# Kernel tuning notes

Measured on AMD Instinct MI355X. Metric: run time of the kernel, lower is better.

Reference implementation:

```python
import jax, jax.numpy as jnp
import numpy as np

N_HEADS = 16
SEG_LEN = 512
MSG_LEN = 1536
T_TOTAL = SEG_LEN + MSG_LEN  # 2048


def _build_mask(T):
    # rows < SEG_LEN: attend to all cols < SEG_LEN (full, non-causal block)
    # rows >= SEG_LEN: standard causal (cols <= row)
    rows = jnp.arange(T)[:, None]
    cols = jnp.arange(T)[None, :]
    mask = jnp.where(rows < SEG_LEN, cols < SEG_LEN, cols <= rows)
    return mask  # [T, T] bool


def setup_inputs() -> dict:
    key = jax.random.key(0)
    k1, k2, k3 = jax.random.split(key, 3)
    B, T, E = 4, T_TOTAL, 1024
    x = jax.random.normal(k1, (B, T, E), dtype=jnp.float32)
    W_qkv = jax.random.normal(k2, (E, 3 * E), dtype=jnp.float32) * (1.0 / np.sqrt(E))
    b_qkv = jnp.zeros((3 * E,), dtype=jnp.float32)
    W_proj = jax.random.normal(k3, (E, E), dtype=jnp.float32) * (1.0 / np.sqrt(E))
    b_proj = jnp.zeros((E,), dtype=jnp.float32)
    return {"x": x, "W_qkv": W_qkv, "b_qkv": b_qkv, "W_proj": W_proj, "b_proj": b_proj}


def reference(x, W_qkv, b_qkv, W_proj, b_proj):
    B, T, E = x.shape
    H = N_HEADS
    D = E // H
    qkv = x @ W_qkv + b_qkv  # [B, T, 3E]
    q, k, v = jnp.split(qkv, 3, axis=-1)
    # [B, H, T, D]
    q = q.reshape(B, T, H, D).transpose(0, 2, 1, 3)
    k = k.reshape(B, T, H, D).transpose(0, 2, 1, 3)
    v = v.reshape(B, T, H, D).transpose(0, 2, 1, 3)
    att = jnp.einsum("bhqd,bhkd->bhqk", q, k) * (1.0 / np.sqrt(D))
    mask = _build_mask(T)  # [T, T]
    att = jnp.where(mask[None, None], att, jnp.float32(-jnp.inf))
    att = jax.nn.softmax(att, axis=-1)
    y = jnp.einsum("bhqk,bhkd->bhqd", att, v)
    y = y.transpose(0, 2, 1, 3).reshape(B, T, E)
    return y @ W_proj + b_proj
```

## Files before the change

kernel.cpp:

```cpp
#include <hip/hip_runtime.h>


typedef _Float16 f16;
typedef _Float16 f16x4 __attribute__((ext_vector_type(4)));
typedef _Float16 f16x8 __attribute__((ext_vector_type(8)));
typedef float f32x4 __attribute__((ext_vector_type(4)));

#define MFMA16x32(a, b, c) __builtin_amdgcn_mfma_f32_16x16x32_f16(a, b, c, 0, 0, 0)
#define MFMA16x16(a, b, c) __builtin_amdgcn_mfma_f32_16x16x16f16(a, b, c, 0, 0, 0)

__device__ __forceinline__ void gload_lds16(const void* g, void* l) {
  __builtin_amdgcn_global_load_lds(
      (__attribute__((address_space(1))) void*)g,
      (__attribute__((address_space(3))) void*)l, 16, 0, 0);
}


__global__ __launch_bounds__(256) void k_prep(
    const float* __restrict__ x, f16* __restrict__ xh,
    const float* __restrict__ Wq, f16* __restrict__ Wqt,
    const float* __restrict__ Wp, f16* __restrict__ Wpt) {
  __shared__ float tile[32][33];
  const int bid = blockIdx.x;
  if (bid < 8192) {
    int i = bid * 256 + threadIdx.x;
    float4 v = ((const float4*)x)[i];
    f16x4 o = {(f16)v.x, (f16)v.y, (f16)v.z, (f16)v.w};
    ((f16x4*)xh)[i] = o;
    return;
  }
  const float* W;
  f16* Wt;
  int Ndim, bx, by;
  if (bid < 8192 + 3072) {
    int r = bid - 8192;
    W = Wq; Wt = Wqt; Ndim = 3072; bx = r % 96; by = r / 96;
  } else {
    int r = bid - 11264;
    W = Wp; Wt = Wpt; Ndim = 1024; bx = r % 32; by = r / 32;
  }
  const int tx = threadIdx.x & 31, ty = threadIdx.x >> 5;
  const int n = bx * 32 + tx;
  const int k0 = by * 32;
  for (int j = ty; j < 32; j += 8)
    tile[j][tx] = W[(size_t)(k0 + j) * Ndim + n];
  __syncthreads();
  const int k = k0 + tx;
  for (int j = ty; j < 32; j += 8)
    Wt[(size_t)(bx * 32 + j) * 1024 + k] = (f16)tile[tx][j];
}


__global__ __launch_bounds__(512, 2) void k_gemm_qkv(
    const f16* __restrict__ A, const f16* __restrict__ Bt,
    const float* __restrict__ bias,
    f16* __restrict__ Qo, f16* __restrict__ Ko, f16* __restrict__ Vo) {
  constexpr int KD = 1024;
  constexpr int SLOT = (128 + 256) * 64;
  __shared__ __align__(16) f16 smem[3 * SLOT];
  const int tid = threadIdx.x;
  const int wave = tid >> 6, lane = tid & 63;
  const int g = lane >> 4, l16 = lane & 15;
  const int m0 = blockIdx.y * 128, n0 = blockIdx.x * 256;
  const int wm = (wave >> 2) * 64, wn = (wave & 3) * 64;
  const int srow = wave * 8 + (lane >> 3);
  const int skc = ((lane & 7) ^ (lane >> 3)) * 8;

  f32x4 acc[4][4] = {};

  for (int t = 0; t < 2; ++t) {
    f16* Sa = smem + t * SLOT;
    f16* Sb = Sa + 128 * 64;
    for (int it = 0; it < 2; ++it)
      gload_lds16(A + (size_t)(m0 + it * 64 + srow) * KD + t * 64 + skc,
                  Sa + (it * 64 + wave * 8) * 64);
    for (int it = 0; it < 4; ++it)
      gload_lds16(Bt + (size_t)(n0 + it * 64 + srow) * KD + t * 64 + skc,
                  Sb + (it * 64 + wave * 8) * 64);
  }
  asm volatile("s_waitcnt vmcnt(6)" ::: "memory");
  __builtin_amdgcn_s_barrier();

  for (int u = 0; u < 16; ++u) {
    const int s = u % 3;
    f16* Sa = smem + s * SLOT;
    f16* Sb = Sa + 128 * 64;
    const bool pf = (u + 2) < 16;
    f16* Pa = smem + ((u + 2) % 3) * SLOT;
    f16* Pb = Pa + 128 * 64;
    const int kp = (u + 2) * 64;

    for (int kk = 0; kk < 2; ++kk) {
      if (pf) {
        if (kk == 0) {
          gload_lds16(A + (size_t)(m0 + srow) * KD + kp + skc,
                      Pa + (wave * 8) * 64);
          gload_lds16(A + (size_t)(m0 + 64 + srow) * KD + kp + skc,
                      Pa + (64 + wave * 8) * 64);
          gload_lds16(Bt + (size_t)(n0 + srow) * KD + kp + skc,
                      Pb + (wave * 8) * 64);
        } else {
          gload_lds16(Bt + (size_t)(n0 + 64 + srow) * KD + kp + skc,
                      Pb + (64 + wave * 8) * 64);
          gload_lds16(Bt + (size_t)(n0 + 128 + srow) * KD + kp + skc,
                      Pb + (128 + wave * 8) * 64);
          gload_lds16(Bt + (size_t)(n0 + 192 + srow) * KD + kp + skc,
                      Pb + (192 + wave * 8) * 64);
        }
      }

      const int ks = kk * 4;
      f16x8 af[4], bf[4];
      for (int mi = 0; mi < 4; ++mi) {
        int R = wm + mi * 16 + l16, sw = R & 7;
        af[mi] = *(const f16x8*)(Sa + R * 64 + ((ks + g) ^ sw) * 8);
      }
      for (int ni = 0; ni < 4; ++ni) {
        int R = wn + ni * 16 + l16, sw = R & 7;
        bf[ni] = *(const f16x8*)(Sb + R * 64 + ((ks + g) ^ sw) * 8);
      }
      __builtin_amdgcn_s_setprio(1);
      for (int mi = 0; mi < 4; ++mi)
        for (int ni = 0; ni < 4; ++ni)
          acc[mi][ni] = MFMA16x32(af[mi], bf[ni], acc[mi][ni]);
      __builtin_amdgcn_s_setprio(0);
    }

    if (u < 14)
      asm volatile("s_waitcnt vmcnt(6)" ::: "memory");
    else
      asm volatile("s_waitcnt vmcnt(0)" ::: "memory");
    __builtin_amdgcn_s_barrier();
  }

  const int nsub = n0 + wn;
  const int part = nsub >> 10;
  const int h    = (nsub >> 6) & 15;
  const int mg   = m0 + wm;
  const int b    = mg >> 11;
  const int tb   = mg & 2047;
  const size_t bh = (size_t)(b * 16 + h);

  float bv[4];
  for (int ni = 0; ni < 4; ++ni) bv[ni] = bias[nsub + ni * 16 + l16];

  f16* Es = smem + wave * 4096;

  for (int mi = 0; mi < 4; ++mi)
    for (int ni = 0; ni < 4; ++ni)
      for (int r = 0; r < 4; ++r) {
        f16 hv = (f16)(acc[mi][ni][r] + bv[ni]);
        int mrow = mi * 16 + g * 4 + r, ncol = ni * 16 + l16;
        if (part == 2)
          Es[ncol * 64 + (mrow ^ ((ncol & 7) << 3))] = hv;
        else
          Es[mrow * 64 + (ncol ^ ((mrow & 7) << 3))] = hv;
      }

  const int rrow = lane >> 3, rj = lane & 7;
  for (int p = 0; p < 8; ++p) {
    int row = p * 8 + rrow;
    f16x8 vv = *(const f16x8*)(Es + row * 64 + (rj ^ (row & 7)) * 8);
    int rcol = rj * 8;
    if (part == 0)
      *(f16x8*)(Qo + (bh * 2048 + tb + row) * 64 + rcol) = vv;
    else if (part == 1)
      *(f16x8*)(Ko + (bh * 2048 + tb + row) * 64 + rcol) = vv;
    else
      *(f16x8*)(Vo + (bh * 64 + row) * 2048 + tb + rcol) = vv;
  }
}


__global__ __launch_bounds__(256, 4) void k_attn(
    const f16* __restrict__ Q, const f16* __restrict__ Kb,
    const f16* __restrict__ Vt, f16* __restrict__ Y) {
  __shared__ __align__(16) f16 Ks[2][64 * 64];
  __shared__ __align__(16) f16 Vs[2][64 * 64];
  __shared__ float rs[4 * 32];

  const int tid = threadIdx.x;
  const int wave = tid >> 6, lane = tid & 63;
  const int g = lane >> 4, l16 = lane & 15;
  const int bh = blockIdx.x;
  const int b = bh >> 4, h = bh & 15;
  const int qt = 15 - blockIdx.y;
  const int q0 = qt * 128;
  const int nt = (qt < 4) ? 8 : (qt + 1) * 2;
  const int srowrel = lane >> 3;
  const int sc = (lane & 7) ^ srowrel;

  const f32x4 sinit = {-8.65617025f, -8.65617025f, -8.65617025f, -8.65617025f};

  f16x8 aq[2][2];
  for (int mi = 0; mi < 2; ++mi) {
    const f16* qrow =
        Q + ((size_t)bh * 2048 + q0 + wave * 32 + mi * 16 + l16) * 64 + g * 8;
    aq[mi][0] = *(const f16x8*)(qrow);
    aq[mi][1] = *(const f16x8*)(qrow + 32);
    for (int kb = 0; kb < 2; ++kb)
      aq[mi][kb] = aq[mi][kb] * (f16)0.18033688f;
  }

  f32x4 o[2][4] = {};
  float rsum[2] = {};

  for (int it = 0; it < 2; ++it) {
    int row = it * 32 + wave * 8 + srowrel;
    gload_lds16(Kb + ((size_t)bh * 2048 + row) * 64 + sc * 8,
                &Ks[0][(it * 32 + wave * 8) * 64]);
    gload_lds16(Vt + ((size_t)bh * 64 + row) * 2048 + sc * 8,
                &Vs[0][(it * 32 + wave * 8) * 64]);
  }
  __syncthreads();

  int cur = 0;
  for (int i = 0; i < nt; ++i) {
    if (i + 1 < nt) {
      const int kn0 = (i + 1) << 6;
      for (int it = 0; it < 2; ++it) {
        int row = it * 32 + wave * 8 + srowrel;
        gload_lds16(Kb + ((size_t)bh * 2048 + kn0 + row) * 64 + sc * 8,
                    &Ks[cur ^ 1][(it * 32 + wave * 8) * 64]);
        gload_lds16(Vt + ((size_t)bh * 64 + row) * 2048 + kn0 + sc * 8,
                    &Vs[cur ^ 1][(it * 32 + wave * 8) * 64]);
      }
    }

    const int kt0 = i << 6;
    const f16* Kc = Ks[cur];
    const f16* Vc = Vs[cur];

    f32x4 t[2][4];
    __builtin_amdgcn_s_setprio(1);
    for (int nb = 0; nb < 4; ++nb) {
      int R = nb * 16 + l16, sw = R & 7;
      f16x8 bk0 = *(const f16x8*)(Kc + R * 64 + ((0 + g) ^ sw) * 8);
      f16x8 bk1 = *(const f16x8*)(Kc + R * 64 + ((4 + g) ^ sw) * 8);
      for (int mi = 0; mi < 2; ++mi) {
        f32x4 acc = MFMA16x32(bk0, aq[mi][0], sinit);
        t[mi][nb] = MFMA16x32(bk1, aq[mi][1], acc);
      }
    }
    __builtin_amdgcn_s_setprio(0);

    const bool masked = (q0 >= 512) && (kt0 >= q0);
    f16x4 ap[4][2];
    for (int mi = 0; mi < 2; ++mi) {
      const int mrow = q0 + wave * 32 + mi * 16 + l16;
      for (int nb = 0; nb < 4; ++nb)
        for (int r = 0; r < 4; ++r) {
          float pv = __builtin_amdgcn_exp2f(t[mi][nb][r]);
          if (masked && (kt0 + nb * 16 + g * 4 + r > mrow)) pv = 0.f;
          rsum[mi] += pv;
          ap[nb][mi][r] = (f16)pv;
        }
    }

    __builtin_amdgcn_s_setprio(1);
    for (int db = 0; db < 4; ++db)
      for (int nb = 0; nb < 4; ++nb) {
        int R = db * 16 + l16, sw = R & 7;
        int c = nb * 2 + (g >> 1);
        f16x4 bv = *(const f16x4*)(Vc + R * 64 + (c ^ sw) * 8 + (g & 1) * 4);
        for (int mi = 0; mi < 2; ++mi)
          o[mi][db] = MFMA16x16(ap[nb][mi], bv, o[mi][db]);
      }
    __builtin_amdgcn_s_setprio(0);

    __syncthreads();
    cur ^= 1;
  }

  for (int mi = 0; mi < 2; ++mi) {
    rsum[mi] += __shfl_xor(rsum[mi], 16, 64);
    rsum[mi] += __shfl_xor(rsum[mi], 32, 64);
  }

  if (g == 0)
    for (int mi = 0; mi < 2; ++mi) rs[wave * 32 + mi * 16 + l16] = rsum[mi];
  float rinv[2][4];
  for (int mi = 0; mi < 2; ++mi)
    for (int r = 0; r < 4; ++r)
      rinv[mi][r] = 1.0f / rs[wave * 32 + mi * 16 + g * 4 + r];

  const size_t ybase = (size_t)b * 2048 + q0 + wave * 32;
  for (int mi = 0; mi < 2; ++mi)
    for (int db = 0; db < 4; ++db)
      for (int r = 0; r < 4; ++r)
        Y[(ybase + mi * 16 + g * 4 + r) * 1024 + h * 64 + db * 16 + l16] =
            (f16)(o[mi][db][r] * rinv[mi][r]);
}


__global__ __launch_bounds__(256) void k_gemm_proj(
    const f16* __restrict__ A, const f16* __restrict__ Bt,
    const float* __restrict__ bias, float* __restrict__ out) {
  constexpr int KD = 1024;
  __shared__ __align__(16) f16 As[128 * 64];
  __shared__ __align__(16) f16 Bs[128 * 64];
  const int tid = threadIdx.x;
  const int wave = tid >> 6, lane = tid & 63;
  const int g = lane >> 4, l16 = lane & 15;
  const int m0 = blockIdx.y * 128, n0 = blockIdx.x * 128;
  const int wm = (wave >> 1) * 64, wn = (wave & 1) * 64;
  const int srow = wave * 8 + (lane >> 3);
  const int skc = ((lane & 7) ^ (lane >> 3)) * 8;

  f32x4 acc[4][4] = {};

  for (int k0 = 0; k0 < KD; k0 += 64) {
    __syncthreads();
    for (int it = 0; it < 4; ++it) {
      gload_lds16(A + (size_t)(m0 + it * 32 + srow) * KD + k0 + skc,
                  As + (it * 32 + wave * 8) * 64);
      gload_lds16(Bt + (size_t)(n0 + it * 32 + srow) * KD + k0 + skc,
                  Bs + (it * 32 + wave * 8) * 64);
    }
    __syncthreads();
    for (int kk = 0; kk < 64; kk += 32) {
      const int ks = kk >> 3;
      f16x8 af[4], bf[4];
      for (int mi = 0; mi < 4; ++mi) {
        int R = wm + mi * 16 + l16, sw = R & 7;
        af[mi] = *(const f16x8*)(As + R * 64 + ((ks + g) ^ sw) * 8);
      }
      for (int ni = 0; ni < 4; ++ni) {
        int R = wn + ni * 16 + l16, sw = R & 7;
        bf[ni] = *(const f16x8*)(Bs + R * 64 + ((ks + g) ^ sw) * 8);
      }
      for (int mi = 0; mi < 4; ++mi)
        for (int ni = 0; ni < 4; ++ni)
          acc[mi][ni] = MFMA16x32(af[mi], bf[ni], acc[mi][ni]);
    }
  }

  float bv[4];
  for (int ni = 0; ni < 4; ++ni) bv[ni] = bias[n0 + wn + ni * 16 + l16];

  for (int mi = 0; mi < 4; ++mi)
    for (int ni = 0; ni < 4; ++ni)
      for (int r = 0; r < 4; ++r) {
        int m = m0 + wm + mi * 16 + g * 4 + r;
        int n = n0 + wn + ni * 16 + l16;
        out[(size_t)m * 1024 + n] = acc[mi][ni][r] + bv[ni];
      }
}


extern "C" void kernel_launch(void* const* d_in, const int* in_sizes, int n_in,
                              void* d_out, int out_size, void* d_ws,
                              size_t ws_size, hipStream_t stream) {
  const float* x      = (const float*)d_in[0];
  const float* W_qkv  = (const float*)d_in[1];
  const float* b_qkv  = (const float*)d_in[2];
  const float* W_proj = (const float*)d_in[3];
  const float* b_proj = (const float*)d_in[4];
  float* out = (float*)d_out;

  char* ws = (char*)d_ws;
  f16* xh    = (f16*)ws;   ws += (size_t)8192 * 1024 * 2;
  f16* Wqt   = (f16*)ws;   ws += (size_t)3072 * 1024 * 2;
  f16* Wpt   = (f16*)ws;   ws += (size_t)1024 * 1024 * 2;
  f16* Qb    = (f16*)ws;   ws += (size_t)64 * 2048 * 64 * 2;
  f16* Kb    = (f16*)ws;   ws += (size_t)64 * 2048 * 64 * 2;
  f16* Vt    = (f16*)ws;   ws += (size_t)64 * 64 * 2048 * 2;
  f16* Y = xh;

  k_prep<<<12288, 256, 0, stream>>>(x, xh, W_qkv, Wqt, W_proj, Wpt);
  k_gemm_qkv<<<dim3(12, 64), 512, 0, stream>>>(xh, Wqt, b_qkv, Qb, Kb, Vt);
  k_attn<<<dim3(64, 16), 256, 0, stream>>>(Qb, Kb, Vt, Y);
  k_gemm_proj<<<dim3(8, 64), 256, 0, stream>>>(Y, Wpt, b_proj, out);
}
```

Measured before the change: 252.2 us.

## Triple-buffer projection GEMM with larger tiles; compute attention row sums via MFMA

The projection GEMM now uses 512-thread blocks on 128x256 tiles. A three-slot LDS ring prefetches two K-steps ahead, with explicit vmcnt waits and a single barrier per step instead of two syncs per step. This is meant to overlap global loads with MFMA work. In attention, the softmax row sums are computed with an MFMA against a ones vector, which removes the scalar adds, the shuffles and the LDS reduction. The cost is 8 extra MFMAs per tile, plus larger shared memory and register use in the GEMM, which may reduce occupancy.

```diff
diff --git a/kernel.cpp b/kernel.cpp
--- a/kernel.cpp
+++ b/kernel.cpp
@@ -177,7 +177,6 @@
     const f16* __restrict__ Vt, f16* __restrict__ Y) {
   __shared__ __align__(16) f16 Ks[2][64 * 64];
   __shared__ __align__(16) f16 Vs[2][64 * 64];
-  __shared__ float rs[4 * 32];
 
   const int tid = threadIdx.x;
   const int wave = tid >> 6, lane = tid & 63;
@@ -191,6 +190,7 @@
   const int sc = (lane & 7) ^ srowrel;
 
   const f32x4 sinit = {-8.65617025f, -8.65617025f, -8.65617025f, -8.65617025f};
+  const f16x4 vone = {(f16)1.f, (f16)1.f, (f16)1.f, (f16)1.f};
 
   f16x8 aq[2][2];
   for (int mi = 0; mi < 2; ++mi) {
@@ -203,7 +203,7 @@
   }
 
   f32x4 o[2][4] = {};
-  float rsum[2] = {};
+  f32x4 rs_acc[2] = {};
 
   for (int it = 0; it < 2; ++it) {
     int row = it * 32 + wave * 8 + srowrel;
@@ -252,12 +252,14 @@
         for (int r = 0; r < 4; ++r) {
           float pv = __builtin_amdgcn_exp2f(t[mi][nb][r]);
           if (masked && (kt0 + nb * 16 + g * 4 + r > mrow)) pv = 0.f;
-          rsum[mi] += pv;
           ap[nb][mi][r] = (f16)pv;
         }
     }
 
     __builtin_amdgcn_s_setprio(1);
+    for (int nb = 0; nb < 4; ++nb)
+      for (int mi = 0; mi < 2; ++mi)
+        rs_acc[mi] = MFMA16x16(ap[nb][mi], vone, rs_acc[mi]);
     for (int db = 0; db < 4; ++db)
       for (int nb = 0; nb < 4; ++nb) {
         int R = db * 16 + l16, sw = R & 7;
@@ -272,17 +274,10 @@
     cur ^= 1;
   }
 
-  for (int mi = 0; mi < 2; ++mi) {
-    rsum[mi] += __shfl_xor(rsum[mi], 16, 64);
-    rsum[mi] += __shfl_xor(rsum[mi], 32, 64);
-  }
-
-  if (g == 0)
-    for (int mi = 0; mi < 2; ++mi) rs[wave * 32 + mi * 16 + l16] = rsum[mi];
   float rinv[2][4];
   for (int mi = 0; mi < 2; ++mi)
     for (int r = 0; r < 4; ++r)
-      rinv[mi][r] = 1.0f / rs[wave * 32 + mi * 16 + g * 4 + r];
+      rinv[mi][r] = 1.0f / rs_acc[mi][r];
 
   const size_t ybase = (size_t)b * 2048 + q0 + wave * 32;
   for (int mi = 0; mi < 2; ++mi)
@@ -293,46 +288,85 @@
 }
 
 
-__global__ __launch_bounds__(256) void k_gemm_proj(
+__global__ __launch_bounds__(512, 2) void k_gemm_proj(
     const f16* __restrict__ A, const f16* __restrict__ Bt,
     const float* __restrict__ bias, float* __restrict__ out) {
   constexpr int KD = 1024;
-  __shared__ __align__(16) f16 As[128 * 64];
-  __shared__ __align__(16) f16 Bs[128 * 64];
+  constexpr int SLOT = (128 + 256) * 64;
+  __shared__ __align__(16) f16 smem[3 * SLOT];
   const int tid = threadIdx.x;
   const int wave = tid >> 6, lane = tid & 63;
   const int g = lane >> 4, l16 = lane & 15;
-  const int m0 = blockIdx.y * 128, n0 = blockIdx.x * 128;
-  const int wm = (wave >> 1) * 64, wn = (wave & 1) * 64;
+  const int m0 = blockIdx.y * 128, n0 = blockIdx.x * 256;
+  const int wm = (wave >> 2) * 64, wn = (wave & 3) * 64;
   const int srow = wave * 8 + (lane >> 3);
   const int skc = ((lane & 7) ^ (lane >> 3)) * 8;
 
   f32x4 acc[4][4] = {};
 
-  for (int k0 = 0; k0 < KD; k0 += 64) {
-    __syncthreads();
-    for (int it = 0; it < 4; ++it) {
-      gload_lds16(A + (size_t)(m0 + it * 32 + srow) * KD + k0 + skc,
-                  As + (it * 32 + wave * 8) * 64);
-      gload_lds16(Bt + (size_t)(n0 + it * 32 + srow) * KD + k0 + skc,
-                  Bs + (it * 32 + wave * 8) * 64);
-    }
-    __syncthreads();
-    for (int kk = 0; kk < 64; kk += 32) {
-      const int ks = kk >> 3;
+  for (int t = 0; t < 2; ++t) {
+    f16* Sa = smem + t * SLOT;
+    f16* Sb = Sa + 128 * 64;
+    for (int it = 0; it < 2; ++it)
+      gload_lds16(A + (size_t)(m0 + it * 64 + srow) * KD + t * 64 + skc,
+                  Sa + (it * 64 + wave * 8) * 64);
+    for (int it = 0; it < 4; ++it)
+      gload_lds16(Bt + (size_t)(n0 + it * 64 + srow) * KD + t * 64 + skc,
+                  Sb + (it * 64 + wave * 8) * 64);
+  }
+  asm volatile("s_waitcnt vmcnt(6)" ::: "memory");
+  __builtin_amdgcn_s_barrier();
+
+  for (int u = 0; u < 16; ++u) {
+    const int s = u % 3;
+    f16* Sa = smem + s * SLOT;
+    f16* Sb = Sa + 128 * 64;
+    const bool pf = (u + 2) < 16;
+    f16* Pa = smem + ((u + 2) % 3) * SLOT;
+    f16* Pb = Pa + 128 * 64;
+    const int kp = (u + 2) * 64;
+
+    for (int kk = 0; kk < 2; ++kk) {
+      if (pf) {
+        if (kk == 0) {
+          gload_lds16(A + (size_t)(m0 + srow) * KD + kp + skc,
+                      Pa + (wave * 8) * 64);
+          gload_lds16(A + (size_t)(m0 + 64 + srow) * KD + kp + skc,
+                      Pa + (64 + wave * 8) * 64);
+          gload_lds16(Bt + (size_t)(n0 + srow) * KD + kp + skc,
+                      Pb + (wave * 8) * 64);
+        } else {
+          gload_lds16(Bt + (size_t)(n0 + 64 + srow) * KD + kp + skc,
+                      Pb + (64 + wave * 8) * 64);
+          gload_lds16(Bt + (size_t)(n0 + 128 + srow) * KD + kp + skc,
+                      Pb + (128 + wave * 8) * 64);
+          gload_lds16(Bt + (size_t)(n0 + 192 + srow) * KD + kp + skc,
+                      Pb + (192 + wave * 8) * 64);
+        }
+      }
+
+      const int ks = kk * 4;
       f16x8 af[4], bf[4];
       for (int mi = 0; mi < 4; ++mi) {
         int R = wm + mi * 16 + l16, sw = R & 7;
-        af[mi] = *(const f16x8*)(As + R * 64 + ((ks + g) ^ sw) * 8);
+        af[mi] = *(const f16x8*)(Sa + R * 64 + ((ks + g) ^ sw) * 8);
       }
       for (int ni = 0; ni < 4; ++ni) {
         int R = wn + ni * 16 + l16, sw = R & 7;
-        bf[ni] = *(const f16x8*)(Bs + R * 64 + ((ks + g) ^ sw) * 8);
-      }
+        bf[ni] = *(const f16x8*)(Sb + R * 64 + ((ks + g) ^ sw) * 8);
+      }
+      __builtin_amdgcn_s_setprio(1);
       for (int mi = 0; mi < 4; ++mi)
         for (int ni = 0; ni < 4; ++ni)
           acc[mi][ni] = MFMA16x32(af[mi], bf[ni], acc[mi][ni]);
+      __builtin_amdgcn_s_setprio(0);
     }
+
+    if (u < 14)
+      asm volatile("s_waitcnt vmcnt(6)" ::: "memory");
+    else
+      asm volatile("s_waitcnt vmcnt(0)" ::: "memory");
+    __builtin_amdgcn_s_barrier();
   }
 
   float bv[4];
@@ -370,5 +404,5 @@
   k_prep<<<12288, 256, 0, stream>>>(x, xh, W_qkv, Wqt, W_proj, Wpt);
   k_gemm_qkv<<<dim3(12, 64), 512, 0, stream>>>(xh, Wqt, b_qkv, Qb, Kb, Vt);
   k_attn<<<dim3(64, 16), 256, 0, stream>>>(Qb, Kb, Vt, Y);
-  k_gemm_proj<<<dim3(8, 64), 256, 0, stream>>>(Y, Wpt, b_proj, out);
-}
+  k_gemm_proj<<<dim3(4, 64), 512, 0, stream>>>(Y, Wpt, b_proj, out);
+}
```

Result: faster. 247.0 us (-2.1%).
